# Performance work log

Measured on AMD Instinct MI355X. Metric: run time of the kernel, lower is better.

Reference implementation:

```python
import jax, jax.numpy as jnp
import numpy as np

N = 1024
IN_F = 256
OUT_F = 128
H = 4
NH = OUT_F // H  # 32
NEG_SLOPE = 0.2


def setup_inputs() -> dict:
    key = jax.random.key(0)
    k1, k2, k3, k4, k5 = jax.random.split(key, 5)
    h = jax.random.normal(k1, (N, IN_F), dtype=jnp.float32)
    adj_mat = jax.random.randint(k2, (N, N, 1), 0, 2, dtype=jnp.int32)
    s_in = 1.0 / np.sqrt(IN_F)
    s_nh = 1.0 / np.sqrt(NH)
    Wl = jax.random.uniform(k3, (H * NH, IN_F), jnp.float32, -s_in, s_in)
    Wr = jax.random.uniform(k4, (H * NH, IN_F), jnp.float32, -s_in, s_in)
    attn_w = jax.random.uniform(k5, (NH,), jnp.float32, -s_nh, s_nh)
    return {"h": h, "adj_mat": adj_mat, "Wl": Wl, "Wr": Wr, "attn_w": attn_w}


def reference(h, adj_mat, Wl, Wr, attn_w):
    n = h.shape[0]
    g_l = (h @ Wl.T).reshape(n, H, NH)  # [N,H,F]
    g_r = (h @ Wr.T).reshape(n, H, NH)  # [N,H,F]
    # g_sum[i, j] = g_l[j] + g_r[i]  (repeat / repeat_interleave semantics)
    g_sum = g_l[None, :, :, :] + g_r[:, None, :, :]  # [N,N,H,F]
    act = jnp.where(g_sum >= 0, g_sum, NEG_SLOPE * g_sum)
    e = jnp.einsum('ijhf,f->ijh', act, attn_w)  # [N,N,H]
    mask = adj_mat != 0  # [N,N,1] broadcasts over heads
    e = jnp.where(mask, e, -jnp.inf)
    a = jax.nn.softmax(e, axis=1)  # softmax over source nodes j
    h_prime = jnp.einsum('ijh,jhf->ihf', a, g_r).reshape(n, H * NH)
    # is_output_layer=False -> ELU (dropout is a no-op in eval)
    return jax.nn.elu(h_prime)
```

## Files before the change

kernel.cpp:

```cpp
#include <hip/hip_runtime.h>
#include <math.h>

#define NN 1024
#define IN_F 256
#define OUT_F 128
#define NHEADS 4
#define NHF 32
#define HPSTR 260

__global__ void __launch_bounds__(256) glr_gemm(const float* __restrict__ hmat,
                                                const float* __restrict__ Wl,
                                                const float* __restrict__ Wr,
                                                float* __restrict__ glh,
                                                float* __restrict__ grh) {
    __shared__ float hp[64 * HPSTR];
    const int tid = threadIdx.x;
    const int rg = blockIdx.x & 15;
    const int cs = blockIdx.x >> 4;

    const float4* __restrict__ hsrc = (const float4*)hmat + rg * (64 * 64);
#pragma unroll
    for (int i = 0; i < 16; ++i) {
        const int v = tid + i * 256;
        const int row = v >> 6, kq = v & 63;
        const float4 x = hsrc[v];
        *(float4*)(hp + row * HPSTR + kq * 4) = x;
    }
    __syncthreads();

    const int lane = tid & 63;
    const int wu = __builtin_amdgcn_readfirstlane(tid >> 6);
    const int c0 = cs * 16 + wu * 4;
    const float* __restrict__ wbase = (c0 < OUT_F) ? (Wl + c0 * IN_F)
                                                   : (Wr + (c0 - OUT_F) * IN_F);
    const float* __restrict__ hrow = hp + lane * HPSTR;

    float a0 = 0.f, a1 = 0.f, a2 = 0.f, a3 = 0.f;
#pragma unroll 4
    for (int kq = 0; kq < 64; ++kq) {
        const float4 hv = *(const float4*)(hrow + kq * 4);
        const float4 w0 = *(const float4*)(wbase + 0 * IN_F + kq * 4);
        const float4 w1 = *(const float4*)(wbase + 1 * IN_F + kq * 4);
        const float4 w2 = *(const float4*)(wbase + 2 * IN_F + kq * 4);
        const float4 w3 = *(const float4*)(wbase + 3 * IN_F + kq * 4);
        a0 = fmaf(hv.x, w0.x, fmaf(hv.y, w0.y, fmaf(hv.z, w0.z, fmaf(hv.w, w0.w, a0))));
        a1 = fmaf(hv.x, w1.x, fmaf(hv.y, w1.y, fmaf(hv.z, w1.z, fmaf(hv.w, w1.w, a1))));
        a2 = fmaf(hv.x, w2.x, fmaf(hv.y, w2.y, fmaf(hv.z, w2.z, fmaf(hv.w, w2.w, a2))));
        a3 = fmaf(hv.x, w3.x, fmaf(hv.y, w3.y, fmaf(hv.z, w3.z, fmaf(hv.w, w3.w, a3))));
    }

    const int row = rg * 64 + lane;
    const int cb = c0 & (OUT_F - 1);
    const int hh = cb >> 5;
    const int f  = cb & 31;
    float* __restrict__ dst = (c0 < OUT_F) ? glh : grh;
    float4 r; r.x = a0; r.y = a1; r.z = a2; r.w = a3;
    *(float4*)(dst + (hh * NN + row) * NHF + f) = r;
}

__global__ void __launch_bounds__(512) gat_main(const float* __restrict__ glh,
                                                const float* __restrict__ grh,
                                                const int* __restrict__ adj,
                                                const float* __restrict__ attn_w,
                                                float* __restrict__ out) {
    const int hh  = blockIdx.y;
    const int i0  = blockIdx.x * 8;
    const int tid = threadIdx.x;

    __shared__ float p_buf[8][1028];
    __shared__ float part[8][16][32];
    __shared__ float red[8][8];
    __shared__ float l_sh[8];

    float lpart[8];
#pragma unroll
    for (int ii = 0; ii < 8; ++ii) lpart[ii] = 0.f;

    for (int c = 0; c < 2; ++c) {
        const int j = (c << 9) + tid;
        const float* __restrict__ gp = glh + (hh * NN + j) * NHF;
        float gl[NHF];
#pragma unroll
        for (int f4 = 0; f4 < 8; ++f4) {
            const float4 v = *(const float4*)(gp + (f4 << 2));
            gl[4 * f4 + 0] = v.x; gl[4 * f4 + 1] = v.y;
            gl[4 * f4 + 2] = v.z; gl[4 * f4 + 3] = v.w;
        }
        float alpha = 0.f;
#pragma unroll
        for (int f = 0; f < NHF; ++f) alpha = fmaf(gl[f], attn_w[f], alpha);
        int adjv[8];
#pragma unroll
        for (int ii = 0; ii < 8; ++ii) adjv[ii] = adj[(i0 + ii) * NN + j];
#pragma unroll
        for (int ii = 0; ii < 8; ++ii) {
            const float* __restrict__ grp = grh + (hh * NN + i0 + ii) * NHF;
            float S0 = 0.f, S1 = 0.f;
#pragma unroll
            for (int f = 0; f < NHF; f += 2) {
                const float s0 = gl[f]     + grp[f];
                const float s1 = gl[f + 1] + grp[f + 1];
                S0 = fmaf(fabsf(s0), attn_w[f],     S0);
                S1 = fmaf(fabsf(s1), attn_w[f + 1], S1);
            }
            const float e = fmaf(0.4f, S0 + S1, 0.6f * alpha);
            const float p = adjv[ii] ? __expf(e) : 0.f;
            p_buf[ii][j] = p;
            lpart[ii] += p;
        }
    }

    const int lane = tid & 63, wv = tid >> 6;
#pragma unroll
    for (int ii = 0; ii < 8; ++ii) {
        float v = lpart[ii];
#pragma unroll
        for (int d = 32; d > 0; d >>= 1) v += __shfl_xor(v, d);
        if (lane == 0) red[ii][wv] = v;
    }
    __syncthreads();
    if (tid < 8) {
        float l = red[tid][0];
#pragma unroll
        for (int w = 1; w < 8; ++w) l += red[tid][w];
        l_sh[tid] = l;
    }
    __syncthreads();

    const int f  = tid & 31;
    const int js = tid >> 5;
    const float* __restrict__ gp = grh + hh * NN * NHF + f;
    float o[8];
#pragma unroll
    for (int ii = 0; ii < 8; ++ii) o[ii] = 0.f;
    const int jb = js << 6;
    for (int jj = 0; jj < 64; jj += 4) {
        const int j = jb + jj;
        const float g0 = gp[(j + 0) * NHF];
        const float g1 = gp[(j + 1) * NHF];
        const float g2 = gp[(j + 2) * NHF];
        const float g3 = gp[(j + 3) * NHF];
#pragma unroll
        for (int ii = 0; ii < 8; ++ii) {
            const float4 p4 = *(const float4*)&p_buf[ii][j];
            o[ii] = fmaf(p4.x, g0, fmaf(p4.y, g1, fmaf(p4.z, g2, fmaf(p4.w, g3, o[ii]))));
        }
    }
#pragma unroll
    for (int ii = 0; ii < 8; ++ii) part[ii][js][f] = o[ii];
    __syncthreads();

    if (tid < 256) {
        const int ii = tid >> 5, ff = tid & 31;
        float s = 0.f;
#pragma unroll
        for (int k = 0; k < 16; ++k) s += part[ii][k][ff];
        s /= l_sh[ii];
        const float r = (s > 0.f) ? s : (__expf(s) - 1.f);
        out[(i0 + ii) * OUT_F + hh * NHF + ff] = r;
    }
}

extern "C" void kernel_launch(void* const* d_in, const int* in_sizes, int n_in,
                              void* d_out, int out_size, void* d_ws, size_t ws_size,
                              hipStream_t stream) {
    const float* hmat = (const float*)d_in[0];
    const int*   adj  = (const int*)d_in[1];
    const float* Wl   = (const float*)d_in[2];
    const float* Wr   = (const float*)d_in[3];
    const float* aw   = (const float*)d_in[4];
    float* o          = (float*)d_out;

    float* glh = (float*)d_ws;
    float* grh = glh + NHEADS * NN * NHF;

    glr_gemm<<<dim3(256), dim3(256), 0, stream>>>(hmat, Wl, Wr, glh, grh);
    gat_main<<<dim3(NN / 8, NHEADS), dim3(512), 0, stream>>>(glh, grh, adj, aw, o);
}
```

Baseline: 101.0 us.

## Restructure projection GEMM to split-K over 4-row tiles without LDS staging

The h-by-W projection kernel is rewritten so each block handles 4 rows and one weight matrix. Each thread computes one output column over half of K and reads W and h straight from global memory, and the two K-halves are combined through a small shared buffer. This drops the 66KB LDS tile and its load phase and launches 512 blocks instead of 256, aiming for better occupancy on the small GEMM. In exchange, every thread streams its own W row, so it depends on cache hits for W, and the output stores become scalar instead of float4.

Measured after the change: 106.1 us. +5.1%, slower.

```diff
diff --git a/kernel.cpp b/kernel.cpp
--- a/kernel.cpp
+++ b/kernel.cpp
@@ -6,56 +6,55 @@
 #define OUT_F 128
 #define NHEADS 4
 #define NHF 32
-#define HPSTR 260
 
 __global__ void __launch_bounds__(256) glr_gemm(const float* __restrict__ hmat,
                                                 const float* __restrict__ Wl,
                                                 const float* __restrict__ Wr,
                                                 float* __restrict__ glh,
                                                 float* __restrict__ grh) {
-    __shared__ float hp[64 * HPSTR];
-    const int tid = threadIdx.x;
-    const int rg = blockIdx.x & 15;
-    const int cs = blockIdx.x >> 4;
+    const int tid  = threadIdx.x;
+    const int r0   = blockIdx.x * 4;
+    const int half = blockIdx.y;
+    const int cl   = tid & 127;
+    const int kh   = tid >> 7;
 
-    const float4* __restrict__ hsrc = (const float4*)hmat + rg * (64 * 64);
-#pragma unroll
-    for (int i = 0; i < 16; ++i) {
-        const int v = tid + i * 256;
-        const int row = v >> 6, kq = v & 63;
-        const float4 x = hsrc[v];
-        *(float4*)(hp + row * HPSTR + kq * 4) = x;
+    const float* __restrict__ W = half ? Wr : Wl;
+    const float4* __restrict__ w4 = (const float4*)(W + cl * IN_F + kh * 128);
+    const float4* __restrict__ h0 = (const float4*)(hmat + (r0 + 0) * IN_F + kh * 128);
+    const float4* __restrict__ h1 = (const float4*)(hmat + (r0 + 1) * IN_F + kh * 128);
+    const float4* __restrict__ h2 = (const float4*)(hmat + (r0 + 2) * IN_F + kh * 128);
+    const float4* __restrict__ h3 = (const float4*)(hmat + (r0 + 3) * IN_F + kh * 128);
+
+    float a0 = 0.f, a1 = 0.f, a2 = 0.f, a3 = 0.f;
+#pragma unroll 8
+    for (int q = 0; q < 32; ++q) {
+        const float4 w  = w4[q];
+        const float4 x0 = h0[q];
+        const float4 x1 = h1[q];
+        const float4 x2 = h2[q];
+        const float4 x3 = h3[q];
+        a0 = fmaf(w.x, x0.x, fmaf(w.y, x0.y, fmaf(w.z, x0.z, fmaf(w.w, x0.w, a0))));
+        a1 = fmaf(w.x, x1.x, fmaf(w.y, x1.y, fmaf(w.z, x1.z, fmaf(w.w, x1.w, a1))));
+        a2 = fmaf(w.x, x2.x, fmaf(w.y, x2.y, fmaf(w.z, x2.z, fmaf(w.w, x2.w, a2))));
+        a3 = fmaf(w.x, x3.x, fmaf(w.y, x3.y, fmaf(w.z, x3.z, fmaf(w.w, x3.w, a3))));
     }
+
+    __shared__ float cmb[2][4][128];
+    cmb[kh][0][cl] = a0;
+    cmb[kh][1][cl] = a1;
+    cmb[kh][2][cl] = a2;
+    cmb[kh][3][cl] = a3;
     __syncthreads();
 
-    const int lane = tid & 63;
-    const int wu = __builtin_amdgcn_readfirstlane(tid >> 6);
-    const int c0 = cs * 16 + wu * 4;
-    const float* __restrict__ wbase = (c0 < OUT_F) ? (Wl + c0 * IN_F)
-                                                   : (Wr + (c0 - OUT_F) * IN_F);
-    const float* __restrict__ hrow = hp + lane * HPSTR;
-
-    float a0 = 0.f, a1 = 0.f, a2 = 0.f, a3 = 0.f;
-#pragma unroll 4
-    for (int kq = 0; kq < 64; ++kq) {
-        const float4 hv = *(const float4*)(hrow + kq * 4);
-        const float4 w0 = *(const float4*)(wbase + 0 * IN_F + kq * 4);
-        const float4 w1 = *(const float4*)(wbase + 1 * IN_F + kq * 4);
-        const float4 w2 = *(const float4*)(wbase + 2 * IN_F + kq * 4);
-        const float4 w3 = *(const float4*)(wbase + 3 * IN_F + kq * 4);
-        a0 = fmaf(hv.x, w0.x, fmaf(hv.y, w0.y, fmaf(hv.z, w0.z, fmaf(hv.w, w0.w, a0))));
-        a1 = fmaf(hv.x, w1.x, fmaf(hv.y, w1.y, fmaf(hv.z, w1.z, fmaf(hv.w, w1.w, a1))));
-        a2 = fmaf(hv.x, w2.x, fmaf(hv.y, w2.y, fmaf(hv.z, w2.z, fmaf(hv.w, w2.w, a2))));
-        a3 = fmaf(hv.x, w3.x, fmaf(hv.y, w3.y, fmaf(hv.z, w3.z, fmaf(hv.w, w3.w, a3))));
+    float* __restrict__ dst = half ? grh : glh;
+#pragma unroll
+    for (int t = 0; t < 2; ++t) {
+        const int idx = tid + t * 256;
+        const int r = idx >> 7, c = idx & 127;
+        const float v = cmb[0][r][c] + cmb[1][r][c];
+        const int hh = c >> 5, f = c & 31;
+        dst[(hh * NN + r0 + r) * NHF + f] = v;
     }
-
-    const int row = rg * 64 + lane;
-    const int cb = c0 & (OUT_F - 1);
-    const int hh = cb >> 5;
-    const int f  = cb & 31;
-    float* __restrict__ dst = (c0 < OUT_F) ? glh : grh;
-    float4 r; r.x = a0; r.y = a1; r.z = a2; r.w = a3;
-    *(float4*)(dst + (hh * NN + row) * NHF + f) = r;
 }
 
 __global__ void __launch_bounds__(512) gat_main(const float* __restrict__ glh,
@@ -174,6 +173,6 @@
     float* glh = (float*)d_ws;
     float* grh = glh + NHEADS * NN * NHF;
 
-    glr_gemm<<<dim3(256), dim3(256), 0, stream>>>(hmat, Wl, Wr, glh, grh);
+    glr_gemm<<<dim3(256, 2), dim3(256), 0, stream>>>(hmat, Wl, Wr, glh, grh);
     gat_main<<<dim3(NN / 8, NHEADS), dim3(512), 0, stream>>>(glh, grh, adj, aw, o);
 }
```
